# Performance work log

Hardware: AMD Instinct MI355X
Metric: run time of the kernel (lower is better)

## Reference

```python
import jax, jax.numpy as jnp
import numpy as np

N_NODES = 50000
N_EDGES = 800000
F_IN = 16
F_EDGE = 8
H = 8  # latent_dim = [8, 8]
NUM_GRAPHS = 512


def setup_inputs() -> dict:
    key = jax.random.key(0)
    ks = jax.random.split(key, 16)
    x = jax.random.normal(ks[0], (N_NODES, F_IN), dtype=jnp.float32)
    edge_index = jax.random.randint(ks[1], (2, N_EDGES), 0, N_NODES)
    edge_attr = jax.random.normal(ks[2], (N_EDGES, F_EDGE), dtype=jnp.float32)
    batch = jnp.sort(jax.random.randint(ks[3], (N_NODES,), 0, NUM_GRAPHS))
    s = 0.1
    # edge MLPs (single Linear each): edge_attr -> flattened [in, out] weight
    We1 = jax.random.normal(ks[4], (F_EDGE, F_IN * H), dtype=jnp.float32) * s
    be1 = jnp.zeros((F_IN * H,), dtype=jnp.float32)
    We2 = jax.random.normal(ks[5], (F_EDGE, H * H), dtype=jnp.float32) * s
    be2 = jnp.zeros((H * H,), dtype=jnp.float32)
    # NNConv root weights + biases
    root1 = jax.random.normal(ks[6], (F_IN, H), dtype=jnp.float32) * s
    b1 = jnp.zeros((H,), dtype=jnp.float32)
    root2 = jax.random.normal(ks[7], (H, H), dtype=jnp.float32) * s
    b2 = jnp.zeros((H,), dtype=jnp.float32)
    # final readout linear H -> 1
    Wlast = jax.random.normal(ks[8], (H, 1), dtype=jnp.float32) * s
    blast = jnp.zeros((1,), dtype=jnp.float32)
    return {"x": x, "edge_index": edge_index, "edge_attr": edge_attr, "batch": batch,
            "We1": We1, "be1": be1, "root1": root1, "b1": b1,
            "We2": We2, "be2": be2, "root2": root2, "b2": b2,
            "Wlast": Wlast, "blast": blast}


def _nnconv(x, src, dst, edge_attr, We, be, root, b, in_dim, out_dim):
    # per-edge weight matrix from edge MLP: [E, in_dim, out_dim]
    W = (edge_attr @ We + be).reshape(-1, in_dim, out_dim)
    # gather source features, per-edge matvec, scatter-add to targets
    msg = jnp.einsum('ei,eio->eo', x[src], W)            # [E, out_dim]
    agg = jax.ops.segment_sum(msg, dst, num_segments=x.shape[0])
    return agg + x @ root + b                            # root weight + bias


def reference(x, edge_index, edge_attr, batch, We1, be1, root1, b1,
              We2, be2, root2, b2, Wlast, blast):
    src, dst = edge_index[0], edge_index[1]
    h = jax.nn.relu(_nnconv(x, src, dst, edge_attr, We1, be1, root1, b1, F_IN, H))
    h = jax.nn.relu(_nnconv(h, src, dst, edge_attr, We2, be2, root2, b2, H, H))
    # per-graph sum pooling (vectorized equivalent of the python loop)
    pooled = jax.ops.segment_sum(h, batch, num_segments=NUM_GRAPHS)  # [G, H]
    return pooled @ Wlast + blast                                    # [G, 1]
```

## Files before the change

### kernel.cpp

```cpp
#include <hip/hip_runtime.h>

#define F_IN 16
#define F_EDGE 8
#define H 8

__global__ void init_out_kernel(float* __restrict__ out,
                                const float* __restrict__ blast, int n) {
    int g = blockIdx.x * blockDim.x + threadIdx.x;
    if (g < n) out[g] = blast[0];
}

__global__ void node_root1_kernel(const float* __restrict__ x,
                                  const float* __restrict__ root1,
                                  const float* __restrict__ b1,
                                  float* __restrict__ h1pre, int n_nodes) {
    int idx = blockIdx.x * blockDim.x + threadIdx.x;
    if (idx >= n_nodes * H) return;
    int n = idx >> 3, j = idx & 7;
    float acc = b1[j];
#pragma unroll
    for (int i = 0; i < F_IN; ++i)
        acc = fmaf(x[n * F_IN + i], root1[i * H + j], acc);
    h1pre[idx] = acc;
}

template <int IN>
__global__ void edge_kernel(const int* __restrict__ ei,
                            const float* __restrict__ ea,
                            const float* __restrict__ feat,
                            const float* __restrict__ We,
                            const float* __restrict__ be,
                            float* __restrict__ agg, int E) {
    constexpr int WSZ = F_EDGE * IN * H;
    __shared__ float sW[WSZ];
    __shared__ float sb[IN * H];
    for (int t = threadIdx.x; t < WSZ; t += blockDim.x) sW[t] = We[t];
    for (int t = threadIdx.x; t < IN * H; t += blockDim.x) sb[t] = be[t];
    __syncthreads();

    long long gid = (long long)blockIdx.x * blockDim.x + threadIdx.x;
    int e = (int)(gid >> 3);
    if (e >= E) return;
    int j = (int)(gid & 7);

    int src = ei[e];
    int dst = ei[E + e];

    float a[F_EDGE];
#pragma unroll
    for (int k = 0; k < F_EDGE; ++k) a[k] = ea[(long long)e * F_EDGE + k];

    float m = 0.f;
#pragma unroll
    for (int i = 0; i < IN; ++i) {
        float w = sb[i * H + j];
#pragma unroll
        for (int k = 0; k < F_EDGE; ++k)
            w = fmaf(a[k], sW[k * (IN * H) + i * H + j], w);
        m = fmaf(feat[(long long)src * IN + i], w, m);
    }
    unsafeAtomicAdd(&agg[(long long)dst * H + j], m);
}

__global__ void relu_root2_kernel(const float* __restrict__ h1pre,
                                  const float* __restrict__ root2,
                                  const float* __restrict__ b2,
                                  float* __restrict__ h1,
                                  float* __restrict__ h2pre, int n_nodes) {
    int idx = blockIdx.x * blockDim.x + threadIdx.x;
    if (idx >= n_nodes * H) return;
    int n = idx >> 3, j = idx & 7;
    float acc = b2[j];
#pragma unroll
    for (int i = 0; i < H; ++i) {
        float hv = h1pre[n * H + i];
        hv = hv > 0.f ? hv : 0.f;
        acc = fmaf(hv, root2[i * H + j], acc);
    }
    float own = h1pre[idx];
    h1[idx] = own > 0.f ? own : 0.f;
    h2pre[idx] = acc;
}

__global__ void pool_kernel(const float* __restrict__ h2pre,
                            const int* __restrict__ batch,
                            const float* __restrict__ Wlast,
                            float* __restrict__ out, int n_nodes) {
    int n = blockIdx.x * blockDim.x + threadIdx.x;
    if (n >= n_nodes) return;
    float c = 0.f;
#pragma unroll
    for (int j = 0; j < H; ++j) {
        float hv = h2pre[n * H + j];
        hv = hv > 0.f ? hv : 0.f;
        c = fmaf(hv, Wlast[j], c);
    }
    unsafeAtomicAdd(&out[batch[n]], c);
}

extern "C" void kernel_launch(void* const* d_in, const int* in_sizes, int n_in,
                              void* d_out, int out_size, void* d_ws, size_t ws_size,
                              hipStream_t stream) {
    const float* x     = (const float*)d_in[0];
    const int*   ei    = (const int*)d_in[1];
    const float* ea    = (const float*)d_in[2];
    const int*   batch = (const int*)d_in[3];
    const float* We1   = (const float*)d_in[4];
    const float* be1   = (const float*)d_in[5];
    const float* root1 = (const float*)d_in[6];
    const float* b1    = (const float*)d_in[7];
    const float* We2   = (const float*)d_in[8];
    const float* be2   = (const float*)d_in[9];
    const float* root2 = (const float*)d_in[10];
    const float* b2    = (const float*)d_in[11];
    const float* Wlast = (const float*)d_in[12];
    const float* blast = (const float*)d_in[13];
    float* out = (float*)d_out;

    int n_nodes = in_sizes[0] / F_IN;
    int E = in_sizes[1] / 2;

    float* h1pre = (float*)d_ws;
    float* h1    = h1pre + (size_t)n_nodes * H;
    float* h2pre = h1 + (size_t)n_nodes * H;

    init_out_kernel<<<(out_size + 255) / 256, 256, 0, stream>>>(out, blast, out_size);

    int nj = n_nodes * H;
    node_root1_kernel<<<(nj + 255) / 256, 256, 0, stream>>>(x, root1, b1, h1pre, n_nodes);

    long long lanes = (long long)E * H;
    int eblks = (int)((lanes + 255) / 256);
    edge_kernel<F_IN><<<eblks, 256, 0, stream>>>(ei, ea, x, We1, be1, h1pre, E);

    relu_root2_kernel<<<(nj + 255) / 256, 256, 0, stream>>>(h1pre, root2, b2, h1, h2pre, n_nodes);

    edge_kernel<H><<<eblks, 256, 0, stream>>>(ei, ea, h1, We2, be2, h2pre, E);

    pool_kernel<<<(n_nodes + 255) / 256, 256, 0, stream>>>(h2pre, batch, Wlast, out, n_nodes);
}
```

Before: 245.7 us.

## Factor edge message into per-node precomputed projections of edge-MLP weights

Reassociates the NNConv message so each node precomputes P[n,j,k]=sum_i f_i We[k,i,j] and q[n,j]=sum_i f_i be[i,j], plus the root term, in a new prep kernel that also fuses the ReLU. Each edge lane then does only an 8-term dot product of edge attributes with the gathered P row, instead of IN*8 FMAs with shared-memory weight reads. This trades edge compute for a larger per-lane random gather (a 32B P row plus q per lane) and a bigger workspace for the P tables.

```diff
diff --git a/kernel.cpp b/kernel.cpp
--- a/kernel.cpp
+++ b/kernel.cpp
@@ -10,34 +10,68 @@
     if (g < n) out[g] = blast[0];
 }
 
-__global__ void node_root1_kernel(const float* __restrict__ x,
-                                  const float* __restrict__ root1,
-                                  const float* __restrict__ b1,
-                                  float* __restrict__ h1pre, int n_nodes) {
-    int idx = blockIdx.x * blockDim.x + threadIdx.x;
-    if (idx >= n_nodes * H) return;
-    int n = idx >> 3, j = idx & 7;
-    float acc = b1[j];
+template <int IN, bool RELU>
+__global__ __launch_bounds__(256) void prep_kernel(
+    const float* __restrict__ feat,
+    const float* __restrict__ We,
+    const float* __restrict__ be,
+    const float* __restrict__ root,
+    const float* __restrict__ b,
+    float* __restrict__ Pt,
+    float* __restrict__ q,
+    float* __restrict__ aggseed,
+    int n_nodes) {
+    __shared__ float sWe[F_EDGE * IN * H];
+    __shared__ float sbe[IN * H];
+    __shared__ float sroot[IN * H];
+    __shared__ float sf[32 * IN];
+
+    int tid = threadIdx.x;
+    for (int t = tid; t < F_EDGE * IN * H; t += 256) sWe[t] = We[t];
+    for (int t = tid; t < IN * H; t += 256) {
+        sbe[t] = be[t];
+        sroot[t] = root[t];
+    }
+    int n0 = blockIdx.x * 32;
+    for (int t = tid; t < 32 * IN; t += 256) {
+        long long g = (long long)n0 * IN + t;
+        float v = (g < (long long)n_nodes * IN) ? feat[g] : 0.f;
+        if (RELU) v = v > 0.f ? v : 0.f;
+        sf[t] = v;
+    }
+    __syncthreads();
+
+    int n = n0 + (tid >> 3);
+    int j = tid & 7;
+    if (n >= n_nodes) return;
+
+    const float* fr = &sf[(tid >> 3) * IN];
+    float p[F_EDGE] = {0.f, 0.f, 0.f, 0.f, 0.f, 0.f, 0.f, 0.f};
+    float qq = 0.f, hr = 0.f;
 #pragma unroll
-    for (int i = 0; i < F_IN; ++i)
-        acc = fmaf(x[n * F_IN + i], root1[i * H + j], acc);
-    h1pre[idx] = acc;
+    for (int i = 0; i < IN; ++i) {
+        float fi = fr[i];
+#pragma unroll
+        for (int k = 0; k < F_EDGE; ++k)
+            p[k] = fmaf(fi, sWe[k * (IN * H) + i * H + j], p[k]);
+        qq = fmaf(fi, sbe[i * H + j], qq);
+        hr = fmaf(fi, sroot[i * H + j], hr);
+    }
+    long long base = ((long long)n * H + j) * F_EDGE;
+    float4* pv = (float4*)(Pt + base);
+    pv[0] = make_float4(p[0], p[1], p[2], p[3]);
+    pv[1] = make_float4(p[4], p[5], p[6], p[7]);
+    q[(long long)n * H + j] = qq;
+    aggseed[(long long)n * H + j] = hr + b[j];
 }
 
-template <int IN>
-__global__ void edge_kernel(const int* __restrict__ ei,
-                            const float* __restrict__ ea,
-                            const float* __restrict__ feat,
-                            const float* __restrict__ We,
-                            const float* __restrict__ be,
-                            float* __restrict__ agg, int E) {
-    constexpr int WSZ = F_EDGE * IN * H;
-    __shared__ float sW[WSZ];
-    __shared__ float sb[IN * H];
-    for (int t = threadIdx.x; t < WSZ; t += blockDim.x) sW[t] = We[t];
-    for (int t = threadIdx.x; t < IN * H; t += blockDim.x) sb[t] = be[t];
-    __syncthreads();
-
+__global__ __launch_bounds__(256) void edge_fact_kernel(
+    const int* __restrict__ ei,
+    const float* __restrict__ ea,
+    const float* __restrict__ Pt,
+    const float* __restrict__ q,
+    float* __restrict__ agg,
+    int E) {
     long long gid = (long long)blockIdx.x * blockDim.x + threadIdx.x;
     int e = (int)(gid >> 3);
     if (e >= E) return;
@@ -46,40 +80,23 @@
     int src = ei[e];
     int dst = ei[E + e];
 
-    float a[F_EDGE];
-#pragma unroll
-    for (int k = 0; k < F_EDGE; ++k) a[k] = ea[(long long)e * F_EDGE + k];
+    const float4* av = (const float4*)(ea + (long long)e * F_EDGE);
+    float4 a0 = av[0], a1 = av[1];
 
-    float m = 0.f;
-#pragma unroll
-    for (int i = 0; i < IN; ++i) {
-        float w = sb[i * H + j];
-#pragma unroll
-        for (int k = 0; k < F_EDGE; ++k)
-            w = fmaf(a[k], sW[k * (IN * H) + i * H + j], w);
-        m = fmaf(feat[(long long)src * IN + i], w, m);
-    }
+    const float4* pv = (const float4*)(Pt + ((long long)src * H + j) * F_EDGE);
+    float4 p0 = pv[0], p1 = pv[1];
+
+    float m = q[(long long)src * H + j];
+    m = fmaf(a0.x, p0.x, m);
+    m = fmaf(a0.y, p0.y, m);
+    m = fmaf(a0.z, p0.z, m);
+    m = fmaf(a0.w, p0.w, m);
+    m = fmaf(a1.x, p1.x, m);
+    m = fmaf(a1.y, p1.y, m);
+    m = fmaf(a1.z, p1.z, m);
+    m = fmaf(a1.w, p1.w, m);
+
     unsafeAtomicAdd(&agg[(long long)dst * H + j], m);
-}
-
-__global__ void relu_root2_kernel(const float* __restrict__ h1pre,
-                                  const float* __restrict__ root2,
-                                  const float* __restrict__ b2,
-                                  float* __restrict__ h1,
-                                  float* __restrict__ h2pre, int n_nodes) {
-    int idx = blockIdx.x * blockDim.x + threadIdx.x;
-    if (idx >= n_nodes * H) return;
-    int n = idx >> 3, j = idx & 7;
-    float acc = b2[j];
-#pragma unroll
-    for (int i = 0; i < H; ++i) {
-        float hv = h1pre[n * H + i];
-        hv = hv > 0.f ? hv : 0.f;
-        acc = fmaf(hv, root2[i * H + j], acc);
-    }
-    float own = h1pre[idx];
-    h1[idx] = own > 0.f ? own : 0.f;
-    h2pre[idx] = acc;
 }
 
 __global__ void pool_kernel(const float* __restrict__ h2pre,
@@ -91,7 +108,7 @@
     float c = 0.f;
 #pragma unroll
     for (int j = 0; j < H; ++j) {
-        float hv = h2pre[n * H + j];
+        float hv = h2pre[(long long)n * H + j];
         hv = hv > 0.f ? hv : 0.f;
         c = fmaf(hv, Wlast[j], c);
     }
@@ -120,22 +137,28 @@
     int n_nodes = in_sizes[0] / F_IN;
     int E = in_sizes[1] / 2;
 
-    float* h1pre = (float*)d_ws;
-    float* h1    = h1pre + (size_t)n_nodes * H;
-    float* h2pre = h1 + (size_t)n_nodes * H;
+    size_t nH = (size_t)n_nodes * H;
+    float* Pt1   = (float*)d_ws;
+    float* q1    = Pt1 + (size_t)n_nodes * H * F_EDGE;
+    float* h1pre = q1 + nH;
+    float* Pt2   = h1pre + nH;
+    float* q2    = Pt2 + (size_t)n_nodes * H * F_EDGE;
+    float* h2pre = q2 + nH;
 
     init_out_kernel<<<(out_size + 255) / 256, 256, 0, stream>>>(out, blast, out_size);
 
-    int nj = n_nodes * H;
-    node_root1_kernel<<<(nj + 255) / 256, 256, 0, stream>>>(x, root1, b1, h1pre, n_nodes);
+    int nblocks = (n_nodes + 31) / 32;
+    prep_kernel<F_IN, false><<<nblocks, 256, 0, stream>>>(
+        x, We1, be1, root1, b1, Pt1, q1, h1pre, n_nodes);
 
     long long lanes = (long long)E * H;
     int eblks = (int)((lanes + 255) / 256);
-    edge_kernel<F_IN><<<eblks, 256, 0, stream>>>(ei, ea, x, We1, be1, h1pre, E);
+    edge_fact_kernel<<<eblks, 256, 0, stream>>>(ei, ea, Pt1, q1, h1pre, E);
 
-    relu_root2_kernel<<<(nj + 255) / 256, 256, 0, stream>>>(h1pre, root2, b2, h1, h2pre, n_nodes);
+    prep_kernel<H, true><<<nblocks, 256, 0, stream>>>(
+        h1pre, We2, be2, root2, b2, Pt2, q2, h2pre, n_nodes);
 
-    edge_kernel<H><<<eblks, 256, 0, stream>>>(ei, ea, h1, We2, be2, h2pre, E);
+    edge_fact_kernel<<<eblks, 256, 0, stream>>>(ei, ea, Pt2, q2, h2pre, E);
 
     pool_kernel<<<(n_nodes + 255) / 256, 256, 0, stream>>>(h2pre, batch, Wlast, out, n_nodes);
 }
```

Result: no change. 242.0 us (-1.5%).
